# Kernel tuning notes

Measured on AMD Instinct MI355X. Metric: run time of the kernel, lower is better.

The kernel has to match this reference:

```python
import jax, jax.numpy as jnp
import numpy as np
import math

B, SQ, SK, D = 32, 2048, 2048, 128


def setup_inputs() -> dict:
    key = jax.random.key(0)
    kq, kk, kv = jax.random.split(key, 3)
    queries = jax.random.normal(kq, (B, SQ, D), dtype=jnp.float32)
    keys = jax.random.normal(kk, (B, SK, D), dtype=jnp.float32)
    values = jax.random.normal(kv, (B, SK, D), dtype=jnp.float32)
    # causal mask: True = masked (future positions), broadcast over batch
    causal = jnp.triu(jnp.ones((SQ, SK), dtype=bool), k=1)
    mask = jnp.broadcast_to(causal, (B, SQ, SK))
    return {"queries": queries, "keys": keys, "values": values, "mask": mask}


def reference(queries, keys, values, mask):
    d = queries.shape[-1]
    scale = 1.0 / math.sqrt(d)
    # [B, Sq, Sk] score matrix (the module materializes this explicitly)
    scores = jnp.einsum("bqd,bkd->bqk", queries, keys) * scale
    scores = jnp.where(mask, -jnp.inf, scores)
    attn = jax.nn.softmax(scores, axis=-1)
    # dropout p=0.0 -> identity (eval parity)
    return jnp.einsum("bqk,bkd->bqd", attn, values)
```

## Files before the change

### kernel.cpp

```cpp
#include <hip/hip_runtime.h>
#include <hip/hip_bf16.h>

#define NB   32
#define SQL  2048
#define DH   128
#define QBLK 128
#define KBLK 64
#define NKT  (SQL / KBLK)
#define TILEB 16384

typedef __attribute__((ext_vector_type(4)))  float f32x4;
typedef __attribute__((ext_vector_type(16))) float f32x16;
typedef __attribute__((ext_vector_type(8)))  short s16x8;
typedef __attribute__((ext_vector_type(4)))  unsigned int u32x4;

__device__ __forceinline__ unsigned int cvtpk_bf16(float lo, float hi) {
  unsigned int r;
  asm("v_cvt_pk_bf16_f32 %0, %1, %2" : "=v"(r) : "v"(lo), "v"(hi));
  return r;
}
#define PLSWAP(x, y) asm volatile("v_permlane32_swap_b32 %0, %1" : "+v"(x), "+v"(y))

__device__ __forceinline__ unsigned int pk2(float lo, float hi) {
  unsigned short a = __builtin_bit_cast(unsigned short, __float2bfloat16(lo));
  unsigned short b = __builtin_bit_cast(unsigned short, __float2bfloat16(hi));
  return (unsigned int)a | ((unsigned int)b << 16);
}

#define AS1(p) ((const __attribute__((address_space(1))) void*)(p))
#define AS3(p) ((__attribute__((address_space(3))) void*)(p))

__global__ __launch_bounds__(256)
void prep_kv(const float* __restrict__ Kg, const float* __restrict__ Vg,
             char* __restrict__ wsK, char* __restrict__ wsV) {
  const int blk = blockIdx.x;
  const int b   = blk >> 5;
  const int kt  = blk & 31;
  const int tid = threadIdx.x;
  const float* Ksrc = Kg + ((size_t)b * SQL + (size_t)kt * KBLK) * DH;
  const float* Vsrc = Vg + ((size_t)b * SQL + (size_t)kt * KBLK) * DH;
  char* Kdst = wsK + (size_t)blk * TILEB;
  char* Vdst = wsV + (size_t)blk * TILEB;

  {
    const int q16 = tid & 15;
    const int r0  = tid >> 4;
    #pragma unroll
    for (int it = 0; it < 4; ++it) {
      const int r = r0 + 16 * it;
      const float* src = Ksrc + (size_t)r * DH + 8 * q16;
      f32x4 a = *(const f32x4*)(src);
      f32x4 d = *(const f32x4*)(src + 4);
      u32x4 w;
      w[0] = pk2(a[0], a[1]); w[1] = pk2(a[2], a[3]);
      w[2] = pk2(d[0], d[1]); w[3] = pk2(d[2], d[3]);
      *(u32x4*)(Kdst + ((r * 256 + 16 * q16) ^ ((r & 7) << 4))) = w;
    }
  }
  {
    const int kq = tid & 15;
    const int dq = tid >> 4;
    #pragma unroll
    for (int it = 0; it < 2; ++it) {
      const int d0 = 4 * dq + 64 * it;
      f32x4 rv[4];
      #pragma unroll
      for (int j = 0; j < 4; ++j)
        rv[j] = *(const f32x4*)(Vsrc + (size_t)(4 * kq + j) * DH + d0);
      #pragma unroll
      for (int j2 = 0; j2 < 4; ++j2) {
        const int dd = d0 + j2;
        uint2 w = make_uint2(pk2(rv[0][j2], rv[1][j2]), pk2(rv[2][j2], rv[3][j2]));
        *(uint2*)(Vdst + ((dd * 128 + 8 * kq) ^ ((dd & 7) << 4))) = w;
      }
    }
  }
}

__global__ __launch_bounds__(256, 2)
void attn_fwd(const float* __restrict__ Qg, const char* __restrict__ wsK,
              const char* __restrict__ wsV, float* __restrict__ Og) {
  __shared__ __align__(16) char smem[65536];

  const int tid  = threadIdx.x;
  const int wid  = tid >> 6;
  const int lane = tid & 63;
  const int hi   = lane >> 5;
  const int c    = lane & 31;

  const int i   = blockIdx.x;
  const int p   = i & 1;
  const int q3  = (i >> 1) & 7;
  const int b   = (i >> 4) & 31;
  const int qtb = (b & 16) ? (15 - q3) : q3;
  const int qt  = p ? qtb : (15 - qtb);
  const int qb  = qt * QBLK;
  const int nt  = 2 * qt + 2;

  const float* Qb = Qg + (size_t)b * SQL * DH;
  float* Ob = Og + (size_t)b * SQL * DH;
  const char* Ktiles = wsK + (size_t)b * NKT * TILEB;
  const char* Vtiles = wsV + (size_t)b * NKT * TILEB;

  const float qscale = 0.08838834764831845f * 1.4426950408889634f;

  s16x8 qf[8];
  {
    const float* qr = Qb + (size_t)(qb + 32*wid + c) * DH + 8*hi;
    #pragma unroll
    for (int ds = 0; ds < 8; ++ds) {
      f32x4 a = *(const f32x4*)(qr + 16*ds);
      f32x4 d = *(const f32x4*)(qr + 16*ds + 4);
      u32x4 w;
      w[0] = pk2(a[0]*qscale, a[1]*qscale);
      w[1] = pk2(a[2]*qscale, a[3]*qscale);
      w[2] = pk2(d[0]*qscale, d[1]*qscale);
      w[3] = pk2(d[2]*qscale, d[3]*qscale);
      qf[ds] = __builtin_bit_cast(s16x8, w);
    }
  }

  f32x16 oacc[4];
  #pragma unroll
  for (int nb = 0; nb < 4; ++nb) oacc[nb] = (f32x16){0.f};
  float m_run = -1e30f, l_run = 0.f;

  const int qglob = qb + 32*wid + c;
  const int qhiw  = qb + 32*wid + 31;
  const int qlow  = qb + 32*wid;

  auto STAGE = [&](int t) {
    const char* ks = Ktiles + (size_t)t * TILEB + tid * 16;
    const char* vs = Vtiles + (size_t)t * TILEB + tid * 16;
    char* kl = smem + (t & 1) * 16384 + wid * 1024;
    char* vl = smem + 32768 + (t & 1) * 16384 + wid * 1024;
    #pragma unroll
    for (int jj = 0; jj < 4; ++jj) {
      __builtin_amdgcn_global_load_lds(AS1(ks + jj * 4096), AS3(kl + jj * 4096), 16, 0, 0);
      __builtin_amdgcn_global_load_lds(AS1(vs + jj * 4096), AS3(vl + jj * 4096), 16, 0, 0);
    }
  };

  STAGE(0);
  STAGE(1);

  for (int t = 0; t < nt; ++t) {
    if (t == nt - 1) asm volatile("s_waitcnt vmcnt(0)" ::: "memory");
    else             asm volatile("s_waitcnt vmcnt(8)" ::: "memory");
    __builtin_amdgcn_s_barrier();
    __builtin_amdgcn_sched_barrier(0);

    const int kb = t * KBLK;
    const char* Kl = smem + (t & 1) * 16384;
    const char* Vl = smem + 32768 + (t & 1) * 16384;

    if (kb <= qhiw) {
      f32x16 sacc[2];
      sacc[0] = (f32x16){0.f};
      sacc[1] = (f32x16){0.f};
      __builtin_amdgcn_s_setprio(1);
      #pragma unroll
      for (int ds = 0; ds < 8; ++ds) {
        #pragma unroll
        for (int mb = 0; mb < 2; ++mb) {
          const int row = 32*mb + c;
          s16x8 kf = *(const s16x8*)(Kl + ((row*256 + 32*ds + 16*hi) ^ ((c & 7) << 4)));
          sacc[mb] = __builtin_amdgcn_mfma_f32_32x32x16_bf16(kf, qf[ds], sacc[mb], 0, 0, 0);
        }
      }
      __builtin_amdgcn_s_setprio(0);

      if (kb + KBLK - 1 > qlow) {
        #pragma unroll
        for (int mb = 0; mb < 2; ++mb)
          #pragma unroll
          for (int r = 0; r < 16; ++r) {
            const int kk = kb + 32*mb + (r & 3) + 8*(r >> 2) + 4*hi;
            if (kk > qglob) sacc[mb][r] = -1e30f;
          }
      }

      float mx[8];
      #pragma unroll
      for (int e = 0; e < 8; ++e)
        mx[e] = fmaxf(fmaxf(sacc[0][e], sacc[0][e+8]), fmaxf(sacc[1][e], sacc[1][e+8]));
      mx[0] = fmaxf(mx[0], mx[4]); mx[1] = fmaxf(mx[1], mx[5]);
      mx[2] = fmaxf(mx[2], mx[6]); mx[3] = fmaxf(mx[3], mx[7]);
      const float tmax = fmaxf(fmaxf(mx[0], mx[1]), fmaxf(mx[2], mx[3]));

      if (!__all(tmax <= m_run + 8.0f)) {
        float tfull = fmaxf(tmax, __shfl_xor(tmax, 32));
        const float mnew  = fmaxf(m_run, tfull);
        const float alpha = exp2f(m_run - mnew);
        #pragma unroll
        for (int r = 0; r < 16; ++r) {
          float av = __shfl(alpha, (r & 3) + 8*(r >> 2) + 4*hi);
          #pragma unroll
          for (int nb = 0; nb < 4; ++nb) oacc[nb][r] *= av;
        }
        l_run *= alpha;
        m_run = mnew;
      }

      float lsa = 0.f, lsb = 0.f;
      unsigned int u0[8], u1[8];
      #pragma unroll
      for (int w = 0; w < 8; ++w) {
        float p0 = exp2f(sacc[0][2*w]     - m_run);
        float p1 = exp2f(sacc[0][2*w + 1] - m_run);
        lsa += p0 + p1;
        u0[w] = cvtpk_bf16(p0, p1);
      }
      #pragma unroll
      for (int w = 0; w < 8; ++w) {
        float p0 = exp2f(sacc[1][2*w]     - m_run);
        float p1 = exp2f(sacc[1][2*w + 1] - m_run);
        lsb += p0 + p1;
        u1[w] = cvtpk_bf16(p0, p1);
      }
      l_run += lsa + lsb;

      PLSWAP(u0[0], u0[2]); PLSWAP(u0[1], u0[3]);
      PLSWAP(u0[4], u0[6]); PLSWAP(u0[5], u0[7]);
      PLSWAP(u1[0], u1[2]); PLSWAP(u1[1], u1[3]);
      PLSWAP(u1[4], u1[6]); PLSWAP(u1[5], u1[7]);
      s16x8 pa[4];
      { u32x4 w = {u0[0], u0[1], u0[2], u0[3]}; pa[0] = __builtin_bit_cast(s16x8, w); }
      { u32x4 w = {u0[4], u0[5], u0[6], u0[7]}; pa[1] = __builtin_bit_cast(s16x8, w); }
      { u32x4 w = {u1[0], u1[1], u1[2], u1[3]}; pa[2] = __builtin_bit_cast(s16x8, w); }
      { u32x4 w = {u1[4], u1[5], u1[6], u1[7]}; pa[3] = __builtin_bit_cast(s16x8, w); }

      __builtin_amdgcn_s_setprio(1);
      #pragma unroll
      for (int nb = 0; nb < 4; ++nb) {
        #pragma unroll
        for (int ks = 0; ks < 4; ++ks) {
          const int row = 32*nb + c;
          s16x8 vf = *(const s16x8*)(Vl + ((row*128 + 32*ks + 16*hi) ^ ((c & 7) << 4)));
          oacc[nb] = __builtin_amdgcn_mfma_f32_32x32x16_bf16(pa[ks], vf, oacc[nb], 0, 0, 0);
        }
      }
      __builtin_amdgcn_s_setprio(0);
    }

    __builtin_amdgcn_s_barrier();
    if (t + 2 < nt) STAGE(t + 2);
  }

  const float l_tot = l_run + __shfl_xor(l_run, 32);
  const float linv  = 1.0f / l_tot;
  float* Orow = Ob + (size_t)(qb + 32*wid) * DH;
  #pragma unroll
  for (int r = 0; r < 16; ++r) {
    const int q = (r & 3) + 8*(r >> 2) + 4*hi;
    float lv = __shfl(linv, q);
    #pragma unroll
    for (int nb = 0; nb < 4; ++nb)
      Orow[(size_t)q * DH + 32*nb + c] = oacc[nb][r] * lv;
  }
}

extern "C" void kernel_launch(void* const* d_in, const int* in_sizes, int n_in,
                              void* d_out, int out_size, void* d_ws, size_t ws_size,
                              hipStream_t stream) {
  const float* Q = (const float*)d_in[0];
  const float* K = (const float*)d_in[1];
  const float* V = (const float*)d_in[2];
  float* O = (float*)d_out;
  char* wsK = (char*)d_ws;
  char* wsV = (char*)d_ws + (size_t)NB * NKT * TILEB;

  prep_kv<<<dim3(NB * NKT), dim3(256), 0, stream>>>(K, V, wsK, wsV);
  attn_fwd<<<dim3(NB * (SQL / QBLK)), dim3(256), 0, stream>>>(Q, wsK, wsV, O);
}
```

Before: 87.95 us.

## Software-pipeline QK^T of next tile with softmax and PV of previous tile

Splits K and V staging into separate async loads and restructures the main loop into a two-stage software pipeline. The QK^T MFMAs of one tile are issued alongside the softmax and PV of the previous tile, so matrix and vector work can overlap. This adds a second score accumulator set, which raises register pressure, and introduces more complex vmcnt and barrier bookkeeping. The per-wave causal skip of tiles is changed: QKT for tile u always runs and SMPV for tiles beyond the causal limit may execute unconditionally, which could add work or affect correctness for waves whose causal limit falls earlier.

```diff
diff --git a/kernel.cpp b/kernel.cpp
--- a/kernel.cpp
+++ b/kernel.cpp
@@ -129,123 +129,148 @@
   const int qhiw  = qb + 32*wid + 31;
   const int qlow  = qb + 32*wid;
 
-  auto STAGE = [&](int t) {
+  auto STAGE_K = [&](int t) {
     const char* ks = Ktiles + (size_t)t * TILEB + tid * 16;
+    char* kl = smem + (t & 1) * 16384 + wid * 1024;
+    #pragma unroll
+    for (int jj = 0; jj < 4; ++jj)
+      __builtin_amdgcn_global_load_lds(AS1(ks + jj*4096), AS3(kl + jj*4096), 16, 0, 0);
+  };
+  auto STAGE_V = [&](int t) {
     const char* vs = Vtiles + (size_t)t * TILEB + tid * 16;
-    char* kl = smem + (t & 1) * 16384 + wid * 1024;
     char* vl = smem + 32768 + (t & 1) * 16384 + wid * 1024;
     #pragma unroll
-    for (int jj = 0; jj < 4; ++jj) {
-      __builtin_amdgcn_global_load_lds(AS1(ks + jj * 4096), AS3(kl + jj * 4096), 16, 0, 0);
-      __builtin_amdgcn_global_load_lds(AS1(vs + jj * 4096), AS3(vl + jj * 4096), 16, 0, 0);
-    }
+    for (int jj = 0; jj < 4; ++jj)
+      __builtin_amdgcn_global_load_lds(AS1(vs + jj*4096), AS3(vl + jj*4096), 16, 0, 0);
   };
 
-  STAGE(0);
-  STAGE(1);
-
-  for (int t = 0; t < nt; ++t) {
-    if (t == nt - 1) asm volatile("s_waitcnt vmcnt(0)" ::: "memory");
-    else             asm volatile("s_waitcnt vmcnt(8)" ::: "memory");
+  auto QKT = [&](int t, f32x16* sacc) {
+    const char* Kl = smem + (t & 1) * 16384;
+    sacc[0] = (f32x16){0.f};
+    sacc[1] = (f32x16){0.f};
+    __builtin_amdgcn_s_setprio(1);
+    #pragma unroll
+    for (int ds = 0; ds < 8; ++ds) {
+      #pragma unroll
+      for (int mb = 0; mb < 2; ++mb) {
+        const int row = 32*mb + c;
+        s16x8 kf = *(const s16x8*)(Kl + ((row*256 + 32*ds + 16*hi) ^ ((c & 7) << 4)));
+        sacc[mb] = __builtin_amdgcn_mfma_f32_32x32x16_bf16(kf, qf[ds], sacc[mb], 0, 0, 0);
+      }
+    }
+    __builtin_amdgcn_s_setprio(0);
+    const int kb = t * KBLK;
+    if (kb + KBLK - 1 > qlow) {
+      #pragma unroll
+      for (int mb = 0; mb < 2; ++mb)
+        #pragma unroll
+        for (int r = 0; r < 16; ++r) {
+          const int kk = kb + 32*mb + (r & 3) + 8*(r >> 2) + 4*hi;
+          if (kk > qglob) sacc[mb][r] = -1e30f;
+        }
+    }
+  };
+
+  auto SMPV = [&](int t, f32x16* sacc) {
+    const char* Vl = smem + 32768 + (t & 1) * 16384;
+
+    float mx[8];
+    #pragma unroll
+    for (int e = 0; e < 8; ++e)
+      mx[e] = fmaxf(fmaxf(sacc[0][e], sacc[0][e+8]), fmaxf(sacc[1][e], sacc[1][e+8]));
+    mx[0] = fmaxf(mx[0], mx[4]); mx[1] = fmaxf(mx[1], mx[5]);
+    mx[2] = fmaxf(mx[2], mx[6]); mx[3] = fmaxf(mx[3], mx[7]);
+    const float tmax = fmaxf(fmaxf(mx[0], mx[1]), fmaxf(mx[2], mx[3]));
+
+    if (!__all(tmax <= m_run + 8.0f)) {
+      float tfull = fmaxf(tmax, __shfl_xor(tmax, 32));
+      const float mnew  = fmaxf(m_run, tfull);
+      const float alpha = exp2f(m_run - mnew);
+      #pragma unroll
+      for (int r = 0; r < 16; ++r) {
+        float av = __shfl(alpha, (r & 3) + 8*(r >> 2) + 4*hi);
+        #pragma unroll
+        for (int nb = 0; nb < 4; ++nb) oacc[nb][r] *= av;
+      }
+      l_run *= alpha;
+      m_run = mnew;
+    }
+
+    float lsa = 0.f, lsb = 0.f;
+    unsigned int u0[8], u1[8];
+    #pragma unroll
+    for (int w = 0; w < 8; ++w) {
+      float p0 = exp2f(sacc[0][2*w]     - m_run);
+      float p1 = exp2f(sacc[0][2*w + 1] - m_run);
+      lsa += p0 + p1;
+      u0[w] = cvtpk_bf16(p0, p1);
+    }
+    #pragma unroll
+    for (int w = 0; w < 8; ++w) {
+      float p0 = exp2f(sacc[1][2*w]     - m_run);
+      float p1 = exp2f(sacc[1][2*w + 1] - m_run);
+      lsb += p0 + p1;
+      u1[w] = cvtpk_bf16(p0, p1);
+    }
+    l_run += lsa + lsb;
+
+    PLSWAP(u0[0], u0[2]); PLSWAP(u0[1], u0[3]);
+    PLSWAP(u0[4], u0[6]); PLSWAP(u0[5], u0[7]);
+    PLSWAP(u1[0], u1[2]); PLSWAP(u1[1], u1[3]);
+    PLSWAP(u1[4], u1[6]); PLSWAP(u1[5], u1[7]);
+    s16x8 pa[4];
+    { u32x4 w = {u0[0], u0[1], u0[2], u0[3]}; pa[0] = __builtin_bit_cast(s16x8, w); }
+    { u32x4 w = {u0[4], u0[5], u0[6], u0[7]}; pa[1] = __builtin_bit_cast(s16x8, w); }
+    { u32x4 w = {u1[0], u1[1], u1[2], u1[3]}; pa[2] = __builtin_bit_cast(s16x8, w); }
+    { u32x4 w = {u1[4], u1[5], u1[6], u1[7]}; pa[3] = __builtin_bit_cast(s16x8, w); }
+
+    __builtin_amdgcn_s_setprio(1);
+    #pragma unroll
+    for (int nb = 0; nb < 4; ++nb) {
+      #pragma unroll
+      for (int ks = 0; ks < 4; ++ks) {
+        const int row = 32*nb + c;
+        s16x8 vf = *(const s16x8*)(Vl + ((row*128 + 32*ks + 16*hi) ^ ((c & 7) << 4)));
+        oacc[nb] = __builtin_amdgcn_mfma_f32_32x32x16_bf16(pa[ks], vf, oacc[nb], 0, 0, 0);
+      }
+    }
+    __builtin_amdgcn_s_setprio(0);
+  };
+
+  STAGE_K(0);
+  STAGE_K(1);
+  STAGE_V(0);
+
+  f32x16 sA[2], sB[2];
+
+  for (int u = 0; u < nt; u += 2) {
+    asm volatile("s_waitcnt vmcnt(8)" ::: "memory");
     __builtin_amdgcn_s_barrier();
     __builtin_amdgcn_sched_barrier(0);
 
-    const int kb = t * KBLK;
-    const char* Kl = smem + (t & 1) * 16384;
-    const char* Vl = smem + 32768 + (t & 1) * 16384;
-
-    if (kb <= qhiw) {
-      f32x16 sacc[2];
-      sacc[0] = (f32x16){0.f};
-      sacc[1] = (f32x16){0.f};
-      __builtin_amdgcn_s_setprio(1);
-      #pragma unroll
-      for (int ds = 0; ds < 8; ++ds) {
-        #pragma unroll
-        for (int mb = 0; mb < 2; ++mb) {
-          const int row = 32*mb + c;
-          s16x8 kf = *(const s16x8*)(Kl + ((row*256 + 32*ds + 16*hi) ^ ((c & 7) << 4)));
-          sacc[mb] = __builtin_amdgcn_mfma_f32_32x32x16_bf16(kf, qf[ds], sacc[mb], 0, 0, 0);
-        }
-      }
-      __builtin_amdgcn_s_setprio(0);
-
-      if (kb + KBLK - 1 > qlow) {
-        #pragma unroll
-        for (int mb = 0; mb < 2; ++mb)
-          #pragma unroll
-          for (int r = 0; r < 16; ++r) {
-            const int kk = kb + 32*mb + (r & 3) + 8*(r >> 2) + 4*hi;
-            if (kk > qglob) sacc[mb][r] = -1e30f;
-          }
-      }
-
-      float mx[8];
-      #pragma unroll
-      for (int e = 0; e < 8; ++e)
-        mx[e] = fmaxf(fmaxf(sacc[0][e], sacc[0][e+8]), fmaxf(sacc[1][e], sacc[1][e+8]));
-      mx[0] = fmaxf(mx[0], mx[4]); mx[1] = fmaxf(mx[1], mx[5]);
-      mx[2] = fmaxf(mx[2], mx[6]); mx[3] = fmaxf(mx[3], mx[7]);
-      const float tmax = fmaxf(fmaxf(mx[0], mx[1]), fmaxf(mx[2], mx[3]));
-
-      if (!__all(tmax <= m_run + 8.0f)) {
-        float tfull = fmaxf(tmax, __shfl_xor(tmax, 32));
-        const float mnew  = fmaxf(m_run, tfull);
-        const float alpha = exp2f(m_run - mnew);
-        #pragma unroll
-        for (int r = 0; r < 16; ++r) {
-          float av = __shfl(alpha, (r & 3) + 8*(r >> 2) + 4*hi);
-          #pragma unroll
-          for (int nb = 0; nb < 4; ++nb) oacc[nb][r] *= av;
-        }
-        l_run *= alpha;
-        m_run = mnew;
-      }
-
-      float lsa = 0.f, lsb = 0.f;
-      unsigned int u0[8], u1[8];
-      #pragma unroll
-      for (int w = 0; w < 8; ++w) {
-        float p0 = exp2f(sacc[0][2*w]     - m_run);
-        float p1 = exp2f(sacc[0][2*w + 1] - m_run);
-        lsa += p0 + p1;
-        u0[w] = cvtpk_bf16(p0, p1);
-      }
-      #pragma unroll
-      for (int w = 0; w < 8; ++w) {
-        float p0 = exp2f(sacc[1][2*w]     - m_run);
-        float p1 = exp2f(sacc[1][2*w + 1] - m_run);
-        lsb += p0 + p1;
-        u1[w] = cvtpk_bf16(p0, p1);
-      }
-      l_run += lsa + lsb;
-
-      PLSWAP(u0[0], u0[2]); PLSWAP(u0[1], u0[3]);
-      PLSWAP(u0[4], u0[6]); PLSWAP(u0[5], u0[7]);
-      PLSWAP(u1[0], u1[2]); PLSWAP(u1[1], u1[3]);
-      PLSWAP(u1[4], u1[6]); PLSWAP(u1[5], u1[7]);
-      s16x8 pa[4];
-      { u32x4 w = {u0[0], u0[1], u0[2], u0[3]}; pa[0] = __builtin_bit_cast(s16x8, w); }
-      { u32x4 w = {u0[4], u0[5], u0[6], u0[7]}; pa[1] = __builtin_bit_cast(s16x8, w); }
-      { u32x4 w = {u1[0], u1[1], u1[2], u1[3]}; pa[2] = __builtin_bit_cast(s16x8, w); }
-      { u32x4 w = {u1[4], u1[5], u1[6], u1[7]}; pa[3] = __builtin_bit_cast(s16x8, w); }
-
-      __builtin_amdgcn_s_setprio(1);
-      #pragma unroll
-      for (int nb = 0; nb < 4; ++nb) {
-        #pragma unroll
-        for (int ks = 0; ks < 4; ++ks) {
-          const int row = 32*nb + c;
-          s16x8 vf = *(const s16x8*)(Vl + ((row*128 + 32*ks + 16*hi) ^ ((c & 7) << 4)));
-          oacc[nb] = __builtin_amdgcn_mfma_f32_32x32x16_bf16(pa[ks], vf, oacc[nb], 0, 0, 0);
-        }
-      }
-      __builtin_amdgcn_s_setprio(0);
-    }
+    QKT(u, sA);
+    if (u > 0) SMPV(u - 1, sB);
 
     __builtin_amdgcn_s_barrier();
-    if (t + 2 < nt) STAGE(t + 2);
-  }
+    if (u + 2 < nt) STAGE_K(u + 2);
+    STAGE_V(u + 1);
+
+    if (u + 2 < nt) asm volatile("s_waitcnt vmcnt(8)" ::: "memory");
+    else            asm volatile("s_waitcnt vmcnt(4)" ::: "memory");
+    __builtin_amdgcn_s_barrier();
+    __builtin_amdgcn_sched_barrier(0);
+
+    if ((u + 1) * KBLK <= qhiw) QKT(u + 1, sB);
+    SMPV(u, sA);
+
+    __builtin_amdgcn_s_barrier();
+    if (u + 3 < nt) STAGE_K(u + 3);
+    if (u + 2 < nt) STAGE_V(u + 2);
+  }
+
+  asm volatile("s_waitcnt vmcnt(0)" ::: "memory");
+  __builtin_amdgcn_s_barrier();
+  if ((nt - 1) * KBLK <= qhiw) SMPV(nt - 1, sB);
 
   const float l_tot = l_run + __shfl_xor(l_run, 32);
   const float linv  = 1.0f / l_tot;
```

Result: no change. 87.33 us (-0.7%).
